# Optimization experiments

Hardware: AMD Instinct MI355X
Metric: run time of the kernel (lower is better)

The kernel has to match this reference:

```python
import jax, jax.numpy as jnp
import numpy as np

V = 32000   # vocab
T = 256     # context len
C = 384     # n_embed
H = 6       # heads
D = 64      # head dim (HEAD_SIZE // NUM_HEADS)
L = 6       # blocks
B = 16      # batch
FF = 4 * C


def setup_inputs() -> dict:
    key = jax.random.key(0)
    ks = jax.random.split(key, 16)
    s = 0.02
    p = {}
    p["x_ids"] = jax.random.randint(ks[0], (B, T), 0, V)
    p["y_ids"] = jax.random.randint(ks[1], (B, T), 0, V)
    p["tok_emb"] = jax.random.normal(ks[2], (V, C), jnp.float32) * s
    p["pos_emb"] = jax.random.normal(ks[3], (T, C), jnp.float32) * s
    p["Wq"] = jax.random.normal(ks[4], (L, H, C, D), jnp.float32) * s
    p["Wk"] = jax.random.normal(ks[5], (L, H, C, D), jnp.float32) * s
    p["Wv"] = jax.random.normal(ks[6], (L, H, C, D), jnp.float32) * s
    p["Wo"] = jax.random.normal(ks[7], (L, H * D, C), jnp.float32) * s
    p["bo"] = jnp.zeros((L, C), jnp.float32)
    p["ln1_s"] = jnp.ones((L, C), jnp.float32)
    p["ln1_b"] = jnp.zeros((L, C), jnp.float32)
    p["ln2_s"] = jnp.ones((L, C), jnp.float32)
    p["ln2_b"] = jnp.zeros((L, C), jnp.float32)
    p["W1"] = jax.random.normal(ks[8], (L, C, FF), jnp.float32) * s
    p["b1"] = jnp.zeros((L, FF), jnp.float32)
    p["W2"] = jax.random.normal(ks[9], (L, FF, C), jnp.float32) * s
    p["b2"] = jnp.zeros((L, C), jnp.float32)
    p["lnf_s"] = jnp.ones((C,), jnp.float32)
    p["lnf_b"] = jnp.zeros((C,), jnp.float32)
    p["Whead"] = jax.random.normal(ks[10], (C, V), jnp.float32) * s
    p["bhead"] = jnp.zeros((V,), jnp.float32)
    return p


def _ln(x, scale, bias, eps=1e-5):
    m = x.mean(-1, keepdims=True)
    v = ((x - m) ** 2).mean(-1, keepdims=True)
    return (x - m) * jax.lax.rsqrt(v + eps) * scale + bias


def reference(x_ids, y_ids, tok_emb, pos_emb, Wq, Wk, Wv, Wo, bo,
              ln1_s, ln1_b, ln2_s, ln2_b, W1, b1, W2, b2,
              lnf_s, lnf_b, Whead, bhead):
    Bq, Tq = x_ids.shape
    x = tok_emb[x_ids] + pos_emb[:Tq]                      # [B,T,C]
    mask = jnp.tril(jnp.ones((Tq, Tq), bool))
    scale = C ** -0.5  # NOTE: original scales by input dim C, not head dim
    for l in range(L):
        h = _ln(x, ln1_s[l], ln1_b[l])
        q = jnp.einsum('btc,hcd->bhtd', h, Wq[l])
        k = jnp.einsum('btc,hcd->bhtd', h, Wk[l])
        v = jnp.einsum('btc,hcd->bhtd', h, Wv[l])
        att = jnp.einsum('bhtd,bhsd->bhts', q, k) * scale
        att = jnp.where(mask, att, -jnp.inf)
        att = jax.nn.softmax(att, axis=-1)
        o = jnp.einsum('bhts,bhsd->bhtd', att, v)
        o = o.transpose(0, 2, 1, 3).reshape(Bq, Tq, H * D)  # concat heads
        x = x + o @ Wo[l] + bo[l]
        h2 = _ln(x, ln2_s[l], ln2_b[l])
        x = x + jax.nn.relu(h2 @ W1[l] + b1[l]) @ W2[l] + b2[l]
    x = _ln(x, lnf_s, lnf_b)
    logits = x @ Whead + bhead                             # [B,T,V]
    logp = jax.nn.log_softmax(logits, axis=-1)
    loss = -jnp.take_along_axis(logp, y_ids[..., None], axis=-1).mean()
    return (logits, loss)
```

## Files before the change

kernel.cpp:

```cpp
#include <hip/hip_runtime.h>

typedef unsigned short u16;
typedef u16   u16x8 __attribute__((ext_vector_type(8)));
typedef short s16x8 __attribute__((ext_vector_type(8)));
typedef float f32x4 __attribute__((ext_vector_type(4)));

#define NV 32000
#define NT 256
#define NC 384
#define NH 6
#define ND 64
#define NL 6
#define NB 16
#define NFF 1536
#define NM (NB*NT)
#define QKVSZ (NB*NH*NT*ND)
#define NSLAB (NV/64)

__device__ __forceinline__ u16 f2bf(float f){
    unsigned x = __builtin_bit_cast(unsigned, f);
    x += 0x7fffu + ((x>>16)&1u);
    return (u16)(x>>16);
}

__device__ __forceinline__ void gload_lds16(const u16* g, u16* l){
    __builtin_amdgcn_global_load_lds((const __attribute__((address_space(1))) unsigned int*)g,
                                     (__attribute__((address_space(3))) unsigned int*)l, 16, 0, 0);
}

__global__ __launch_bounds__(256) void embed_ln(const int* __restrict__ ids,
        const float* __restrict__ tok, const float* __restrict__ pos,
        const float* __restrict__ sc, const float* __restrict__ bi,
        float* __restrict__ x, u16* __restrict__ out){
    int row  = blockIdx.x*4 + (threadIdx.x>>6);
    int lane = threadIdx.x & 63;
    int t = row & (NT-1);
    const float* tr = tok + (size_t)ids[row]*NC;
    const float* pr = pos + (size_t)t*NC;
    float* xr = x + (size_t)row*NC;
    float v[6]; float sum = 0.f, sq = 0.f;
    #pragma unroll
    for (int i=0;i<6;++i){
        int c = lane+64*i;
        v[i] = tr[c] + pr[c];
        xr[c] = v[i];
        sum += v[i]; sq += v[i]*v[i];
    }
    #pragma unroll
    for (int off=1; off<64; off<<=1){ sum += __shfl_xor(sum,off); sq += __shfl_xor(sq,off); }
    float mean = sum*(1.f/NC);
    float rstd = rsqrtf(sq*(1.f/NC) - mean*mean + 1e-5f);
    u16* orow = out + (size_t)row*NC;
    #pragma unroll
    for (int i=0;i<6;++i){ int c = lane+64*i; orow[c] = f2bf((v[i]-mean)*rstd*sc[c] + bi[c]); }
}

__global__ __launch_bounds__(256) void ln_kernel(const float* __restrict__ x,
        const float* __restrict__ sc, const float* __restrict__ bi, u16* __restrict__ out){
    int row  = blockIdx.x*4 + (threadIdx.x>>6);
    int lane = threadIdx.x & 63;
    const float* xr = x + (size_t)row*NC;
    float v[6]; float sum = 0.f, sq = 0.f;
    #pragma unroll
    for (int i=0;i<6;++i){ v[i]=xr[lane+64*i]; sum+=v[i]; sq+=v[i]*v[i]; }
    #pragma unroll
    for (int off=1; off<64; off<<=1){ sum += __shfl_xor(sum,off); sq += __shfl_xor(sq,off); }
    float mean = sum*(1.f/NC);
    float rstd = rsqrtf(sq*(1.f/NC) - mean*mean + 1e-5f);
    u16* orow = out + (size_t)row*NC;
    #pragma unroll
    for (int i=0;i<6;++i){ int c = lane+64*i; orow[c] = f2bf((v[i]-mean)*rstd*sc[c] + bi[c]); }
}

struct TDesc {
    const float* in; u16* out;
    int Cc; int nx; int perZ; int obDiv; int oStride; int start;
    long inBatch; long oS1; long oS2; float scale;
};
struct TPack { TDesc d[7]; };

__global__ __launch_bounds__(256) void tconv_all(TPack p){
    __shared__ float tile[32][33];
    int bid = blockIdx.x;
    int e = 0;
    #pragma unroll
    for (int i=1;i<7;++i) e += (bid >= p.d[i].start) ? 1 : 0;
    TDesc D = p.d[e];
    int local = bid - D.start;
    int bz  = local / D.perZ; int rem = local - bz*D.perZ;
    int cy  = rem / D.nx;     int cx  = rem - cy*D.nx;
    int r0 = cy*32, c0 = cx*32;
    const float* ib = D.in + (size_t)bz*D.inBatch;
    u16* ob = D.out + (size_t)(bz/D.obDiv)*D.oS1 + (size_t)(bz%D.obDiv)*D.oS2;
    int tx = threadIdx.x & 31, ty = threadIdx.x >> 5;
    #pragma unroll
    for (int i=0;i<4;++i) tile[ty+8*i][tx] = ib[(size_t)(r0+ty+8*i)*D.Cc + (c0+tx)];
    __syncthreads();
    #pragma unroll
    for (int i=0;i<4;++i) ob[(size_t)(c0+ty+8*i)*D.oStride + (r0+tx)] = f2bf(tile[tx][ty+8*i]*D.scale);
}

template<int EPI, int BM, int BN, int SWZ>
__global__ __launch_bounds__(256,4) void gemm_bt(
        const u16* __restrict__ A, const u16* __restrict__ Bt,
        const float* __restrict__ bias, float* __restrict__ resid,
        u16* __restrict__ outb, float* __restrict__ outf, float* __restrict__ lpart,
        int M, int N, int K){
    constexpr int WM = BM/2, WN = BN/2, MI = WM/16, NI = WN/16;
    __shared__ u16 As[2*BM*32];
    __shared__ u16 Bs[2*BN*32];
    int tid = threadIdx.x;
    int lane = tid & 63, wid = tid >> 6;
    int wm = wid >> 1, wn = wid & 1;
    int l15 = lane & 15, lg = lane >> 4;
    int bx, by;
    if (SWZ){
        int nwg = gridDim.x*gridDim.y;
        int orig = blockIdx.y*gridDim.x + blockIdx.x;
        int swz = (orig&7)*(nwg>>3) + (orig>>3);
        by = swz & 31;
        bx = swz >> 5;
    } else { bx = blockIdx.x; by = blockIdx.y; }
    int m0 = by * BM, n0 = bx * BN;
    f32x4 acc[MI][NI];
    #pragma unroll
    for (int a=0;a<MI;++a)
        #pragma unroll
        for (int b=0;b<NI;++b) acc[a][b] = f32x4{0.f,0.f,0.f,0.f};

    int nk = K >> 6;
    for (int kk = 0; kk < nk; ++kk){
        int k0 = kk << 6;
        #pragma unroll
        for (int h=0;h<2;++h){
            if constexpr (BM >= 64){
                #pragma unroll
                for (int i=0;i<BM/64;++i){
                    int o   = i*4096 + tid*16;
                    int row = o >> 6;
                    int kb  = (o & 63) >> 1;
                    gload_lds16(A + (size_t)(m0+row)*K + (k0+h*32+kb), &As[h*BM*32 + (o>>1)]);
                }
            } else {
                if (tid < BM*4){
                    int o = tid*16;
                    int row = o >> 6;
                    int kb  = (o & 63) >> 1;
                    gload_lds16(A + (size_t)(m0+row)*K + (k0+h*32+kb), &As[h*BM*32 + (o>>1)]);
                }
            }
            #pragma unroll
            for (int i=0;i<BN/64;++i){
                int o   = i*4096 + tid*16;
                int row = o >> 6;
                int kb  = (o & 63) >> 1;
                gload_lds16(Bt + (size_t)(n0+row)*K + (k0+h*32+kb), &Bs[h*BN*32 + (o>>1)]);
            }
        }
        asm volatile("s_waitcnt vmcnt(0)" ::: "memory");
        __syncthreads();
        #pragma unroll
        for (int ks=0;ks<2;++ks){
            s16x8 af[MI];
            #pragma unroll
            for (int mi=0;mi<MI;++mi) af[mi] = *(const s16x8*)&As[ks*BM*32 + (wm*WM+mi*16+l15)*32 + lg*8];
            #pragma unroll
            for (int ni=0;ni<NI;++ni){
                s16x8 bfr = *(const s16x8*)&Bs[ks*BN*32 + (wn*WN+ni*16+l15)*32 + lg*8];
                #pragma unroll
                for (int mi=0;mi<MI;++mi)
                    acc[mi][ni] = __builtin_amdgcn_mfma_f32_16x16x32_bf16(af[mi], bfr, acc[mi][ni], 0,0,0);
            }
        }
        __syncthreads();
    }

    if (EPI == 3){
        float es[MI][4];
        #pragma unroll
        for (int mi=0;mi<MI;++mi)
            #pragma unroll
            for (int r=0;r<4;++r) es[mi][r] = 0.f;
        #pragma unroll
        for (int mi=0;mi<MI;++mi)
            #pragma unroll
            for (int ni=0;ni<NI;++ni)
                #pragma unroll
                for (int r=0;r<4;++r){
                    int mg = m0 + wm*WM + mi*16 + lg*4 + r;
                    int ng = n0 + wn*WN + ni*16 + l15;
                    float val = acc[mi][ni][r] + bias[ng];
                    outf[(size_t)mg*N + ng] = val;
                    es[mi][r] += __expf(val);
                }
        #pragma unroll
        for (int mi=0;mi<MI;++mi)
            #pragma unroll
            for (int r=0;r<4;++r){
                float s = es[mi][r];
                s += __shfl_xor(s,1); s += __shfl_xor(s,2);
                s += __shfl_xor(s,4); s += __shfl_xor(s,8);
                if (l15 == 0){
                    int mg = m0 + wm*WM + mi*16 + lg*4 + r;
                    lpart[(size_t)mg*NSLAB + bx*2 + wn] = s;
                }
            }
        return;
    }

    #pragma unroll
    for (int mi=0;mi<MI;++mi){
        #pragma unroll
        for (int ni=0;ni<NI;++ni){
            #pragma unroll
            for (int r=0;r<4;++r){
                int mg = m0 + wm*WM + mi*16 + lg*4 + r;
                int ng = n0 + wn*WN + ni*16 + l15;
                float c = acc[mi][ni][r];
                if (EPI == 0){
                    int which = ng / NC; int hd = ng - which*NC;
                    int hh = hd >> 6, d = hd & 63;
                    int bb = mg >> 8, tt = mg & (NT-1);
                    outb[(size_t)which*QKVSZ + ((size_t)(bb*NH+hh)*NT + tt)*ND + d] = f2bf(c);
                } else if (EPI == 1){
                    float* pp = resid + (size_t)mg*N + ng;
                    *pp = *pp + c + bias[ng];
                } else if (EPI == 2){
                    outb[(size_t)mg*N + ng] = f2bf(fmaxf(c + bias[ng], 0.f));
                }
            }
        }
    }
}

__global__ __launch_bounds__(256,2) void attn_kernel(const u16* __restrict__ qkv, u16* __restrict__ o){
    int blk = blockIdx.x;
    int qt = blk & 3, bh = blk >> 2;
    int b = bh / NH, h = bh - b*NH;
    int tid = threadIdx.x, lane = tid & 63, w = tid >> 6;
    int l15 = lane & 15, lg = lane >> 4;
    __shared__ u16 Ks[256*72];
    __shared__ u16 Vt[64*264];
    __shared__ u16 Ps[4][16*72];
    const u16* qb = qkv + (size_t)bh*NT*ND;
    const u16* kb = qb + QKVSZ;
    const u16* vb = kb + QKVSZ;
    int nit = (qt+1)*2;
    for (int it=0; it<nit; ++it){
        int idx = it*256 + tid;
        int e0 = idx*8;
        int row = e0 >> 6, col = e0 & 63;
        *(u16x8*)&Ks[row*72+col] = *(const u16x8*)(kb + e0);
        u16x8 vv = *(const u16x8*)(vb + e0);
        #pragma unroll
        for (int j=0;j<8;++j) Vt[(col+j)*264 + row] = vv[j];
    }
    const u16* qrow = qb + (size_t)(qt*64 + w*16 + l15)*ND;
    s16x8 qf[2];
    qf[0] = *(const s16x8*)(qrow + lg*8);
    qf[1] = *(const s16x8*)(qrow + 32 + lg*8);
    __syncthreads();

    f32x4 oacc[4]; float l_[4];
    #pragma unroll
    for (int c=0;c<4;++c){ oacc[c]=f32x4{0.f,0.f,0.f,0.f}; l_[c]=0.f; }
    u16* Pw = &Ps[w][0];

    for (int kt=0; kt<=qt; ++kt){
        f32x4 sacc[4];
        #pragma unroll
        for (int c=0;c<4;++c) sacc[c]=f32x4{0.f,0.f,0.f,0.f};
        #pragma unroll
        for (int ks=0;ks<2;++ks){
            s16x8 kf[4];
            #pragma unroll
            for (int ni=0;ni<4;++ni)
                kf[ni] = *(const s16x8*)&Ks[(kt*64+ni*16+l15)*72 + ks*32 + lg*8];
            #pragma unroll
            for (int ni=0;ni<4;++ni)
                sacc[ni] = __builtin_amdgcn_mfma_f32_16x16x32_bf16(qf[ks], kf[ni], sacc[ni], 0,0,0);
        }
        if (kt == qt){
            #pragma unroll
            for (int ni=0;ni<4;++ni)
                #pragma unroll
                for (int r=0;r<4;++r)
                    if (ni*16+l15 > w*16+lg*4+r) sacc[ni][r] = -1e30f;
        }
        #pragma unroll
        for (int r=0;r<4;++r){
            float rs = 0.f;
            #pragma unroll
            for (int ni=0;ni<4;++ni){
                float p = __expf(sacc[ni][r]);
                sacc[ni][r] = p;
                rs += p;
                Pw[(lg*4+r)*72 + ni*16 + l15] = f2bf(p);
            }
            rs += __shfl_xor(rs,1); rs += __shfl_xor(rs,2);
            rs += __shfl_xor(rs,4); rs += __shfl_xor(rs,8);
            l_[r] += rs;
        }
        #pragma unroll
        for (int ks=0;ks<2;++ks){
            s16x8 pf, vf[4];
            pf = *(const s16x8*)&Pw[l15*72 + ks*32 + lg*8];
            #pragma unroll
            for (int ni=0;ni<4;++ni)
                vf[ni] = *(const s16x8*)&Vt[(ni*16+l15)*264 + kt*64 + ks*32 + lg*8];
            #pragma unroll
            for (int ni=0;ni<4;++ni)
                oacc[ni] = __builtin_amdgcn_mfma_f32_16x16x32_bf16(pf, vf[ni], oacc[ni], 0,0,0);
        }
    }
    #pragma unroll
    for (int ni=0;ni<4;++ni)
        #pragma unroll
        for (int r=0;r<4;++r){
            int t = qt*64 + w*16 + lg*4 + r;
            int d = ni*16 + l15;
            o[((size_t)(b*NT + t))*NC + h*ND + d] = f2bf(oacc[ni][r] / l_[r]);
        }
}

__global__ __launch_bounds__(256) void loss_rows2(const float* __restrict__ lpart,
        const float* __restrict__ logits, const int* __restrict__ y, float* __restrict__ rowloss){
    int row  = blockIdx.x*4 + (threadIdx.x>>6);
    int lane = threadIdx.x & 63;
    const float* pr = lpart + (size_t)row*NSLAB;
    float s = 0.f;
    for (int i = lane; i < NSLAB; i += 64) s += pr[i];
    #pragma unroll
    for (int off=1; off<64; off<<=1) s += __shfl_xor(s, off);
    if (lane==0)
        rowloss[row] = logf(s) - logits[(size_t)row*NV + y[row]];
}

__global__ __launch_bounds__(256) void loss_final(const float* __restrict__ rowloss, float* __restrict__ out){
    int tid = threadIdx.x;
    float s = 0.f;
    for (int i = tid; i < NM; i += 256) s += rowloss[i];
    #pragma unroll
    for (int off=1; off<64; off<<=1) s += __shfl_xor(s, off);
    __shared__ float ss[4];
    if ((tid&63)==0) ss[tid>>6]=s;
    __syncthreads();
    if (tid==0) out[0] = (ss[0]+ss[1]+ss[2]+ss[3]) * (1.f/NM);
}

extern "C" void kernel_launch(void* const* d_in, const int* in_sizes, int n_in,
                              void* d_out, int out_size, void* d_ws, size_t ws_size,
                              hipStream_t stream){
    const int*   x_ids = (const int*)  d_in[0];
    const int*   y_ids = (const int*)  d_in[1];
    const float* tok   = (const float*)d_in[2];
    const float* pos   = (const float*)d_in[3];
    const float* Wq    = (const float*)d_in[4];
    const float* Wk    = (const float*)d_in[5];
    const float* Wv    = (const float*)d_in[6];
    const float* Wo    = (const float*)d_in[7];
    const float* bo    = (const float*)d_in[8];
    const float* ln1s  = (const float*)d_in[9];
    const float* ln1b  = (const float*)d_in[10];
    const float* ln2s  = (const float*)d_in[11];
    const float* ln2b  = (const float*)d_in[12];
    const float* W1    = (const float*)d_in[13];
    const float* b1    = (const float*)d_in[14];
    const float* W2    = (const float*)d_in[15];
    const float* b2    = (const float*)d_in[16];
    const float* lnfs  = (const float*)d_in[17];
    const float* lnfb  = (const float*)d_in[18];
    const float* Wh    = (const float*)d_in[19];
    const float* bh    = (const float*)d_in[20];

    float* logits = (float*)d_out;
    float* lossp  = logits + (size_t)NM*NV;

    char* ws = (char*)d_ws;
    auto alloc = [&](size_t bytes)->char*{ char* p = ws; ws += (bytes + 255) & ~(size_t)255; return p; };
    float* xf    = (float*)alloc((size_t)NM*NC*4);
    u16*   hbf   = (u16*)  alloc((size_t)NM*NC*2);
    u16*   qkvb  = (u16*)  alloc((size_t)3*QKVSZ*2);
    u16*   obf   = (u16*)  alloc((size_t)NM*NC*2);
    u16*   f1bf  = (u16*)  alloc((size_t)NM*NFF*2);
    u16*   qkvw  = (u16*)  alloc((size_t)NL*1152*NC*2);
    u16*   wot   = (u16*)  alloc((size_t)NL*NC*NC*2);
    u16*   w1t   = (u16*)  alloc((size_t)NL*NFF*NC*2);
    u16*   w2t   = (u16*)  alloc((size_t)NL*NC*NFF*2);
    u16*   wht   = (u16*)  alloc((size_t)NV*NC*2);
    float* part  = (float*)alloc((size_t)NM*4);
    float* lpart = (float*)qkvb;

    const float qscale = 0.051031036307982884f;

    TPack tp;
    tp.d[0] = {Wq, qkvw + 0*(NC*NC), ND,  2,  24, NH, NC, 0,     (long)NC*ND, (long)1152*NC, (long)ND*NC, qscale};
    tp.d[1] = {Wk, qkvw + 1*(NC*NC), ND,  2,  24, NH, NC, 864,   (long)NC*ND, (long)1152*NC, (long)ND*NC, 1.f};
    tp.d[2] = {Wv, qkvw + 2*(NC*NC), ND,  2,  24, NH, NC, 1728,  (long)NC*ND, (long)1152*NC, (long)ND*NC, 1.f};
    tp.d[3] = {Wo, wot,              NC, 12, 144, 1,  NC, 2592,  (long)NC*NC, (long)NC*NC,   0,           1.f};
    tp.d[4] = {W1, w1t,             NFF, 48, 576, 1,  NC, 3456,  (long)NC*NFF,(long)NFF*NC,  0,           1.f};
    tp.d[5] = {W2, w2t,              NC, 12, 576, 1, NFF, 6912,  (long)NFF*NC,(long)NC*NFF,  0,           1.f};
    tp.d[6] = {Wh, wht,              NV,1000,12000,1, NC, 10368, 0,           0,             0,           1.f};
    tconv_all<<<22368,256,0,stream>>>(tp);

    embed_ln<<<NM/4,256,0,stream>>>(x_ids, tok, pos, ln1s, ln1b, xf, hbf);
    for (int l = 0; l < NL; ++l){
        gemm_bt<0,64,128,0><<<dim3(1152/128, NM/64),256,0,stream>>>(hbf, qkvw + (size_t)l*1152*NC,
                nullptr, nullptr, qkvb, nullptr, nullptr, NM, 1152, NC);
        attn_kernel<<<NB*NH*4,256,0,stream>>>(qkvb, obf);
        gemm_bt<1,32,128,0><<<dim3(NC/128, NM/32),256,0,stream>>>(obf, wot + (size_t)l*NC*NC,
                bo + l*NC, xf, nullptr, nullptr, nullptr, NM, NC, NC);
        ln_kernel<<<NM/4,256,0,stream>>>(xf, ln2s + l*NC, ln2b + l*NC, hbf);
        gemm_bt<2,64,128,0><<<dim3(NFF/128, NM/64),256,0,stream>>>(hbf, w1t + (size_t)l*NFF*NC,
                b1 + l*NFF, nullptr, f1bf, nullptr, nullptr, NM, NFF, NC);
        gemm_bt<1,32,128,0><<<dim3(NC/128, NM/32),256,0,stream>>>(f1bf, w2t + (size_t)l*NC*NFF,
                b2 + l*NC, xf, nullptr, nullptr, nullptr, NM, NC, NFF);
        if (l < NL-1)
            ln_kernel<<<NM/4,256,0,stream>>>(xf, ln1s + (l+1)*NC, ln1b + (l+1)*NC, hbf);
        else
            ln_kernel<<<NM/4,256,0,stream>>>(xf, lnfs, lnfb, hbf);
    }
    gemm_bt<3,128,128,1><<<dim3(NV/128, NM/128),256,0,stream>>>(hbf, wht, bh,
            nullptr, nullptr, logits, lpart, NM, NV, NC);
    loss_rows2<<<NM/4,256,0,stream>>>(lpart, logits, y_ids, part);
    loss_final<<<1,256,0,stream>>>(part, lossp);
}
```

Measured before the change: 756.9 us.

## Double-buffer GEMM K-loop so global-to-LDS loads overlap MFMA compute

The GEMM main loop now prefetches the next 32-wide K slice into the alternate LDS buffer while the current slice is consumed, using partial vmcnt waits instead of a full drain each iteration. Previously each 64-wide K step loaded both halves, waited for all loads, then computed, which serialized memory latency with MFMA work. The change halves the K step, so there are twice as many barriers per tile, and it depends on exact vmcnt counts per wave being correct, including the case where BM < 64 and only some waves issue A loads.

New measurement: 774.1 us. +2.3%, slower.

```diff
diff --git a/kernel.cpp b/kernel.cpp
--- a/kernel.cpp
+++ b/kernel.cpp
@@ -28,6 +28,20 @@
                                      (__attribute__((address_space(3))) unsigned int*)l, 16, 0, 0);
 }
 
+template<int N> __device__ __forceinline__ void wait_vm(){
+    static_assert(N>=0 && N<=4, "add literal");
+    if constexpr (N==0) asm volatile("s_waitcnt vmcnt(0)" ::: "memory");
+    if constexpr (N==1) asm volatile("s_waitcnt vmcnt(1)" ::: "memory");
+    if constexpr (N==2) asm volatile("s_waitcnt vmcnt(2)" ::: "memory");
+    if constexpr (N==3) asm volatile("s_waitcnt vmcnt(3)" ::: "memory");
+    if constexpr (N==4) asm volatile("s_waitcnt vmcnt(4)" ::: "memory");
+}
+__device__ __forceinline__ void bar(){
+    asm volatile("" ::: "memory");
+    __builtin_amdgcn_s_barrier();
+    asm volatile("" ::: "memory");
+}
+
 __global__ __launch_bounds__(256) void embed_ln(const int* __restrict__ ids,
         const float* __restrict__ tok, const float* __restrict__ pos,
         const float* __restrict__ sc, const float* __restrict__ bi,
@@ -107,8 +121,8 @@
         u16* __restrict__ outb, float* __restrict__ outf, float* __restrict__ lpart,
         int M, int N, int K){
     constexpr int WM = BM/2, WN = BN/2, MI = WM/16, NI = WN/16;
-    __shared__ u16 As[2*BM*32];
-    __shared__ u16 Bs[2*BN*32];
+    __shared__ u16 As[2][BM*32];
+    __shared__ u16 Bs[2][BN*32];
     int tid = threadIdx.x;
     int lane = tid & 63, wid = tid >> 6;
     int wm = wid >> 1, wn = wid & 1;
@@ -128,51 +142,56 @@
         #pragma unroll
         for (int b=0;b<NI;++b) acc[a][b] = f32x4{0.f,0.f,0.f,0.f};
 
-    int nk = K >> 6;
-    for (int kk = 0; kk < nk; ++kk){
-        int k0 = kk << 6;
-        #pragma unroll
-        for (int h=0;h<2;++h){
-            if constexpr (BM >= 64){
-                #pragma unroll
-                for (int i=0;i<BM/64;++i){
-                    int o   = i*4096 + tid*16;
-                    int row = o >> 6;
-                    int kb  = (o & 63) >> 1;
-                    gload_lds16(A + (size_t)(m0+row)*K + (k0+h*32+kb), &As[h*BM*32 + (o>>1)]);
-                }
-            } else {
-                if (tid < BM*4){
-                    int o = tid*16;
-                    int row = o >> 6;
-                    int kb  = (o & 63) >> 1;
-                    gload_lds16(A + (size_t)(m0+row)*K + (k0+h*32+kb), &As[h*BM*32 + (o>>1)]);
-                }
-            }
-            #pragma unroll
-            for (int i=0;i<BN/64;++i){
+    auto STAGE = [&](int kt, int buf){
+        int k0 = kt << 5;
+        if constexpr (BM >= 64){
+            #pragma unroll
+            for (int i=0;i<BM/64;++i){
                 int o   = i*4096 + tid*16;
                 int row = o >> 6;
                 int kb  = (o & 63) >> 1;
-                gload_lds16(Bt + (size_t)(n0+row)*K + (k0+h*32+kb), &Bs[h*BN*32 + (o>>1)]);
+                gload_lds16(A + (size_t)(m0+row)*K + (k0+kb), &As[buf][o>>1]);
             }
-        }
-        asm volatile("s_waitcnt vmcnt(0)" ::: "memory");
-        __syncthreads();
-        #pragma unroll
-        for (int ks=0;ks<2;++ks){
-            s16x8 af[MI];
-            #pragma unroll
-            for (int mi=0;mi<MI;++mi) af[mi] = *(const s16x8*)&As[ks*BM*32 + (wm*WM+mi*16+l15)*32 + lg*8];
-            #pragma unroll
-            for (int ni=0;ni<NI;++ni){
-                s16x8 bfr = *(const s16x8*)&Bs[ks*BN*32 + (wn*WN+ni*16+l15)*32 + lg*8];
-                #pragma unroll
-                for (int mi=0;mi<MI;++mi)
-                    acc[mi][ni] = __builtin_amdgcn_mfma_f32_16x16x32_bf16(af[mi], bfr, acc[mi][ni], 0,0,0);
+        } else {
+            if (tid < BM*4){
+                int o = tid*16;
+                int row = o >> 6;
+                int kb  = (o & 63) >> 1;
+                gload_lds16(A + (size_t)(m0+row)*K + (k0+kb), &As[buf][o>>1]);
             }
         }
-        __syncthreads();
+        #pragma unroll
+        for (int i=0;i<BN/64;++i){
+            int o   = i*4096 + tid*16;
+            int row = o >> 6;
+            int kb  = (o & 63) >> 1;
+            gload_lds16(Bt + (size_t)(n0+row)*K + (k0+kb), &Bs[buf][o>>1]);
+        }
+    };
+
+    int nk = K >> 5;
+    STAGE(0, 0);
+    for (int t = 0; t < nk; ++t){
+        int buf = t & 1;
+        if (t+1 < nk){
+            STAGE(t+1, buf^1);
+            if constexpr (BM >= 64) wait_vm<(BM+BN)/64>();
+            else { if (wid < 2) wait_vm<1+BN/64>(); else wait_vm<BN/64>(); }
+        } else {
+            wait_vm<0>();
+        }
+        bar();
+        s16x8 af[MI];
+        #pragma unroll
+        for (int mi=0;mi<MI;++mi) af[mi] = *(const s16x8*)&As[buf][(wm*WM+mi*16+l15)*32 + lg*8];
+        #pragma unroll
+        for (int ni=0;ni<NI;++ni){
+            s16x8 bfr = *(const s16x8*)&Bs[buf][(wn*WN+ni*16+l15)*32 + lg*8];
+            #pragma unroll
+            for (int mi=0;mi<MI;++mi)
+                acc[mi][ni] = __builtin_amdgcn_mfma_f32_16x16x32_bf16(af[mi], bfr, acc[mi][ni], 0,0,0);
+        }
+        bar();
     }
 
     if (EPI == 3){
```

## Fuse LayerNorm into GEMM prologue using per-row stats from residual epilogues

Applied to the files above, without the earlier changes.

Removes the standalone LayerNorm kernels. The residual-add GEMM epilogues now emit per-row partial sum and sum-of-squares into a small stats buffer, and the consuming GEMMs normalise fp32 activations on the fly while filling LDS as bf16. This drops the bf16 normalised-activation round trip and 13 kernel launches. The cost is that A tiles are now loaded synchronously through registers from fp32 (twice the bytes) instead of by async global-to-LDS, and the stats use a single-pass variance. That is a notable burden on the large vocab head GEMM, which rereads fp32 rows for every column tile.

Result: slower. 902.2 us (+19.2%).

```diff
diff --git a/kernel.cpp b/kernel.cpp
--- a/kernel.cpp
+++ b/kernel.cpp
@@ -28,48 +28,29 @@
                                      (__attribute__((address_space(3))) unsigned int*)l, 16, 0, 0);
 }
 
-__global__ __launch_bounds__(256) void embed_ln(const int* __restrict__ ids,
+__global__ __launch_bounds__(256) void embed_stats(const int* __restrict__ ids,
         const float* __restrict__ tok, const float* __restrict__ pos,
-        const float* __restrict__ sc, const float* __restrict__ bi,
-        float* __restrict__ x, u16* __restrict__ out){
+        float* __restrict__ x, float* __restrict__ statp){
     int row  = blockIdx.x*4 + (threadIdx.x>>6);
     int lane = threadIdx.x & 63;
     int t = row & (NT-1);
     const float* tr = tok + (size_t)ids[row]*NC;
     const float* pr = pos + (size_t)t*NC;
     float* xr = x + (size_t)row*NC;
-    float v[6]; float sum = 0.f, sq = 0.f;
+    float sum = 0.f, sq = 0.f;
     #pragma unroll
     for (int i=0;i<6;++i){
         int c = lane+64*i;
-        v[i] = tr[c] + pr[c];
-        xr[c] = v[i];
-        sum += v[i]; sq += v[i]*v[i];
+        float v = tr[c] + pr[c];
+        xr[c] = v;
+        sum += v; sq += v*v;
     }
     #pragma unroll
     for (int off=1; off<64; off<<=1){ sum += __shfl_xor(sum,off); sq += __shfl_xor(sq,off); }
-    float mean = sum*(1.f/NC);
-    float rstd = rsqrtf(sq*(1.f/NC) - mean*mean + 1e-5f);
-    u16* orow = out + (size_t)row*NC;
-    #pragma unroll
-    for (int i=0;i<6;++i){ int c = lane+64*i; orow[c] = f2bf((v[i]-mean)*rstd*sc[c] + bi[c]); }
-}
-
-__global__ __launch_bounds__(256) void ln_kernel(const float* __restrict__ x,
-        const float* __restrict__ sc, const float* __restrict__ bi, u16* __restrict__ out){
-    int row  = blockIdx.x*4 + (threadIdx.x>>6);
-    int lane = threadIdx.x & 63;
-    const float* xr = x + (size_t)row*NC;
-    float v[6]; float sum = 0.f, sq = 0.f;
-    #pragma unroll
-    for (int i=0;i<6;++i){ v[i]=xr[lane+64*i]; sum+=v[i]; sq+=v[i]*v[i]; }
-    #pragma unroll
-    for (int off=1; off<64; off<<=1){ sum += __shfl_xor(sum,off); sq += __shfl_xor(sq,off); }
-    float mean = sum*(1.f/NC);
-    float rstd = rsqrtf(sq*(1.f/NC) - mean*mean + 1e-5f);
-    u16* orow = out + (size_t)row*NC;
-    #pragma unroll
-    for (int i=0;i<6;++i){ int c = lane+64*i; orow[c] = f2bf((v[i]-mean)*rstd*sc[c] + bi[c]); }
+    if (lane == 0){
+        float* pp = statp + (size_t)row*6;
+        pp[0]=sum; pp[1]=sq; pp[2]=0.f; pp[3]=0.f; pp[4]=0.f; pp[5]=0.f;
+    }
 }
 
 struct TDesc {
@@ -100,15 +81,21 @@
     for (int i=0;i<4;++i) ob[(size_t)(c0+ty+8*i)*D.oStride + (r0+tx)] = f2bf(tile[tx][ty+8*i]*D.scale);
 }
 
-template<int EPI, int BM, int BN, int SWZ>
+template<int EPI, int BM, int BN, int SWZ, int ALN>
 __global__ __launch_bounds__(256,4) void gemm_bt(
-        const u16* __restrict__ A, const u16* __restrict__ Bt,
+        const u16* __restrict__ A, const float* __restrict__ Axf,
+        const u16* __restrict__ Bt,
         const float* __restrict__ bias, float* __restrict__ resid,
         u16* __restrict__ outb, float* __restrict__ outf, float* __restrict__ lpart,
+        const float* __restrict__ statp, float* __restrict__ stout,
+        const float* __restrict__ lnsc, const float* __restrict__ lnbi,
         int M, int N, int K){
     constexpr int WM = BM/2, WN = BN/2, MI = WM/16, NI = WN/16;
+    constexpr int ACH = (BM>=64) ? BM/64 : 1;
     __shared__ u16 As[2*BM*32];
     __shared__ u16 Bs[2*BN*32];
+    __shared__ float stM[ALN?BM:1], stR[ALN?BM:1];
+    __shared__ float sS[2][16][2], sQ[2][16][2];
     int tid = threadIdx.x;
     int lane = tid & 63, wid = tid >> 6;
     int wm = wid >> 1, wn = wid & 1;
@@ -122,6 +109,25 @@
         bx = swz >> 5;
     } else { bx = blockIdx.x; by = blockIdx.y; }
     int m0 = by * BM, n0 = bx * BN;
+
+    float muA[ACH], rsA[ACH];
+    if constexpr (ALN){
+        if (tid < BM){
+            const float* pp = statp + (size_t)(m0+tid)*6;
+            float s = pp[0]+pp[2]+pp[4];
+            float q = pp[1]+pp[3]+pp[5];
+            float mu = s*(1.f/NC);
+            stM[tid] = mu;
+            stR[tid] = rsqrtf(q*(1.f/NC) - mu*mu + 1e-5f);
+        }
+        __syncthreads();
+        #pragma unroll
+        for (int i=0;i<ACH;++i){
+            int row = (i*4096 + tid*16) >> 6;
+            muA[i] = stM[row]; rsA[i] = stR[row];
+        }
+    }
+
     f32x4 acc[MI][NI];
     #pragma unroll
     for (int a=0;a<MI;++a)
@@ -133,7 +139,29 @@
         int k0 = kk << 6;
         #pragma unroll
         for (int h=0;h<2;++h){
-            if constexpr (BM >= 64){
+            if constexpr (ALN){
+                #pragma unroll
+                for (int i=0;i<ACH;++i){
+                    int o   = i*4096 + tid*16;
+                    int row = o >> 6;
+                    int kb  = (o & 63) >> 1;
+                    int kc  = k0 + h*32 + kb;
+                    const float* xr = Axf + (size_t)(m0+row)*K + kc;
+                    float4 v0 = *(const float4*)xr;
+                    float4 v1 = *(const float4*)(xr+4);
+                    float4 s0 = *(const float4*)(lnsc+kc);
+                    float4 s1 = *(const float4*)(lnsc+kc+4);
+                    float4 b0 = *(const float4*)(lnbi+kc);
+                    float4 b1 = *(const float4*)(lnbi+kc+4);
+                    float mu = muA[i], rr = rsA[i];
+                    u16x8 w;
+                    w[0]=f2bf((v0.x-mu)*rr*s0.x+b0.x); w[1]=f2bf((v0.y-mu)*rr*s0.y+b0.y);
+                    w[2]=f2bf((v0.z-mu)*rr*s0.z+b0.z); w[3]=f2bf((v0.w-mu)*rr*s0.w+b0.w);
+                    w[4]=f2bf((v1.x-mu)*rr*s1.x+b1.x); w[5]=f2bf((v1.y-mu)*rr*s1.y+b1.y);
+                    w[6]=f2bf((v1.z-mu)*rr*s1.z+b1.z); w[7]=f2bf((v1.w-mu)*rr*s1.w+b1.w);
+                    *(u16x8*)&As[h*BM*32 + (o>>1)] = w;
+                }
+            } else if constexpr (BM >= 64){
                 #pragma unroll
                 for (int i=0;i<BM/64;++i){
                     int o   = i*4096 + tid*16;
@@ -205,6 +233,38 @@
                     lpart[(size_t)mg*NSLAB + bx*2 + wn] = s;
                 }
             }
+        return;
+    }
+
+    if (EPI == 1){
+        float rs[4]={0.f,0.f,0.f,0.f}, rq[4]={0.f,0.f,0.f,0.f};
+        #pragma unroll
+        for (int ni=0;ni<NI;++ni)
+            #pragma unroll
+            for (int r=0;r<4;++r){
+                int mg = m0 + wm*WM + lg*4 + r;
+                int ng = n0 + wn*WN + ni*16 + l15;
+                float* pp = resid + (size_t)mg*N + ng;
+                float val = acc[0][ni][r] + bias[ng] + *pp;
+                *pp = val;
+                rs[r] += val; rq[r] += val*val;
+            }
+        #pragma unroll
+        for (int r=0;r<4;++r){
+            rs[r]+=__shfl_xor(rs[r],1); rq[r]+=__shfl_xor(rq[r],1);
+            rs[r]+=__shfl_xor(rs[r],2); rq[r]+=__shfl_xor(rq[r],2);
+            rs[r]+=__shfl_xor(rs[r],4); rq[r]+=__shfl_xor(rq[r],4);
+            rs[r]+=__shfl_xor(rs[r],8); rq[r]+=__shfl_xor(rq[r],8);
+            if (l15==0){ sS[wm][lg*4+r][wn]=rs[r]; sQ[wm][lg*4+r][wn]=rq[r]; }
+        }
+        __syncthreads();
+        if (tid < 32){
+            int wmi = tid>>4, rr = tid&15;
+            float s = sS[wmi][rr][0] + sS[wmi][rr][1];
+            float q = sQ[wmi][rr][0] + sQ[wmi][rr][1];
+            float* pp = stout + (size_t)(m0+tid)*6 + bx*2;
+            pp[0]=s; pp[1]=q;
+        }
         return;
     }
 
@@ -222,9 +282,6 @@
                     int hh = hd >> 6, d = hd & 63;
                     int bb = mg >> 8, tt = mg & (NT-1);
                     outb[(size_t)which*QKVSZ + ((size_t)(bb*NH+hh)*NT + tt)*ND + d] = f2bf(c);
-                } else if (EPI == 1){
-                    float* pp = resid + (size_t)mg*N + ng;
-                    *pp = *pp + c + bias[ng];
                 } else if (EPI == 2){
                     outb[(size_t)mg*N + ng] = f2bf(fmaxf(c + bias[ng], 0.f));
                 }
@@ -379,7 +436,7 @@
     char* ws = (char*)d_ws;
     auto alloc = [&](size_t bytes)->char*{ char* p = ws; ws += (bytes + 255) & ~(size_t)255; return p; };
     float* xf    = (float*)alloc((size_t)NM*NC*4);
-    u16*   hbf   = (u16*)  alloc((size_t)NM*NC*2);
+    float* statp = (float*)alloc((size_t)NM*6*4);
     u16*   qkvb  = (u16*)  alloc((size_t)3*QKVSZ*2);
     u16*   obf   = (u16*)  alloc((size_t)NM*NC*2);
     u16*   f1bf  = (u16*)  alloc((size_t)NM*NFF*2);
@@ -403,25 +460,30 @@
     tp.d[6] = {Wh, wht,              NV,1000,12000,1, NC, 10368, 0,           0,             0,           1.f};
     tconv_all<<<22368,256,0,stream>>>(tp);
 
-    embed_ln<<<NM/4,256,0,stream>>>(x_ids, tok, pos, ln1s, ln1b, xf, hbf);
+    embed_stats<<<NM/4,256,0,stream>>>(x_ids, tok, pos, xf, statp);
     for (int l = 0; l < NL; ++l){
-        gemm_bt<0,64,128,0><<<dim3(1152/128, NM/64),256,0,stream>>>(hbf, qkvw + (size_t)l*1152*NC,
-                nullptr, nullptr, qkvb, nullptr, nullptr, NM, 1152, NC);
+        gemm_bt<0,64,128,0,1><<<dim3(1152/128, NM/64),256,0,stream>>>(
+                nullptr, xf, qkvw + (size_t)l*1152*NC,
+                nullptr, nullptr, qkvb, nullptr, nullptr,
+                statp, nullptr, ln1s + l*NC, ln1b + l*NC, NM, 1152, NC);
         attn_kernel<<<NB*NH*4,256,0,stream>>>(qkvb, obf);
-        gemm_bt<1,32,128,0><<<dim3(NC/128, NM/32),256,0,stream>>>(obf, wot + (size_t)l*NC*NC,
-                bo + l*NC, xf, nullptr, nullptr, nullptr, NM, NC, NC);
-        ln_kernel<<<NM/4,256,0,stream>>>(xf, ln2s + l*NC, ln2b + l*NC, hbf);
-        gemm_bt<2,64,128,0><<<dim3(NFF/128, NM/64),256,0,stream>>>(hbf, w1t + (size_t)l*NFF*NC,
-                b1 + l*NFF, nullptr, f1bf, nullptr, nullptr, NM, NFF, NC);
-        gemm_bt<1,32,128,0><<<dim3(NC/128, NM/32),256,0,stream>>>(f1bf, w2t + (size_t)l*NC*NFF,
-                b2 + l*NC, xf, nullptr, nullptr, nullptr, NM, NC, NFF);
-        if (l < NL-1)
-            ln_kernel<<<NM/4,256,0,stream>>>(xf, ln1s + (l+1)*NC, ln1b + (l+1)*NC, hbf);
-        else
-            ln_kernel<<<NM/4,256,0,stream>>>(xf, lnfs, lnfb, hbf);
-    }
-    gemm_bt<3,128,128,1><<<dim3(NV/128, NM/128),256,0,stream>>>(hbf, wht, bh,
-            nullptr, nullptr, logits, lpart, NM, NV, NC);
+        gemm_bt<1,32,128,0,0><<<dim3(NC/128, NM/32),256,0,stream>>>(
+                obf, nullptr, wot + (size_t)l*NC*NC,
+                bo + l*NC, xf, nullptr, nullptr, nullptr,
+                nullptr, statp, nullptr, nullptr, NM, NC, NC);
+        gemm_bt<2,64,128,0,1><<<dim3(NFF/128, NM/64),256,0,stream>>>(
+                nullptr, xf, w1t + (size_t)l*NFF*NC,
+                b1 + l*NFF, nullptr, f1bf, nullptr, nullptr,
+                statp, nullptr, ln2s + l*NC, ln2b + l*NC, NM, NFF, NC);
+        gemm_bt<1,32,128,0,0><<<dim3(NC/128, NM/32),256,0,stream>>>(
+                f1bf, nullptr, w2t + (size_t)l*NC*NFF,
+                b2 + l*NC, xf, nullptr, nullptr, nullptr,
+                nullptr, statp, nullptr, nullptr, NM, NC, NFF);
+    }
+    gemm_bt<3,128,128,1,1><<<dim3(NV/128, NM/128),256,0,stream>>>(
+            nullptr, xf, wht,
+            bh, nullptr, nullptr, logits, lpart,
+            statp, nullptr, lnfs, lnfb, NM, NV, NC);
     loss_rows2<<<NM/4,256,0,stream>>>(lpart, logits, y_ids, part);
     loss_final<<<1,256,0,stream>>>(part, lossp);
 }
```
